# Kernel tuning notes

Hardware: AMD Instinct MI355X
Metric: run time of the kernel (lower is better)

Reference implementation:

```python
import jax, jax.numpy as jnp
import numpy as np

NUM_HEADS = 12
HEAD_DIM = 64
HIDDEN = NUM_HEADS * HEAD_DIM
SCALE = 1.0 / float(np.sqrt(HEAD_DIM))


def _split_heads(x):
    # x: [b, d, s, hidden] -> [b, h, d, s, head_dim]  (transpose_for_scores)
    b, d, s, _ = x.shape
    return jnp.transpose(x.reshape(b, d, s, NUM_HEADS, HEAD_DIM), (0, 3, 1, 2, 4))


def _merge_heads(x):
    # [b, h, d, s, e] -> [b, d, s, hidden]  (untranspose_for_scores)
    b, h, d, s, e = x.shape
    return jnp.transpose(x, (0, 2, 3, 1, 4)).reshape(b, d, s, h * e)


def _segment_attention(q, keys, values, masks, num_docs):
    # _cat_forward: broadcast every key/value/mask list entry to num_docs along
    # dim 2, concat along key length, then scaled-dot-product attention.
    b, h = q.shape[0], q.shape[1]
    q = jnp.broadcast_to(q, (b, h, num_docs, q.shape[3], q.shape[4]))
    k = jnp.concatenate([jnp.broadcast_to(t, (b, h, num_docs, t.shape[3], t.shape[4])) for t in keys], axis=3)
    v = jnp.concatenate([jnp.broadcast_to(t, (b, h, num_docs, t.shape[3], t.shape[4])) for t in values], axis=3)
    mask = jnp.concatenate([jnp.broadcast_to(m, (b, 1, num_docs, 1, m.shape[-1])) for m in masks], axis=-1)
    scores = jnp.einsum('bhdqe,bhdke->bhdqk', q, k) * SCALE + mask
    probs = jax.nn.softmax(scores, axis=-1)
    ctx = jnp.einsum('bhdqk,bhdke->bhdqe', probs, v)
    return _merge_heads(ctx)


def setup_inputs() -> dict:
    key = jax.random.key(0)
    ks = jax.random.split(key, 8)
    B, D, Q, S = 2, 16, 32, 512
    inp = {
        'cls': jax.random.normal(ks[0], (B, 1, 1, HIDDEN), jnp.float32),
        'query': jax.random.normal(ks[1], (B, 1, Q, HIDDEN), jnp.float32),
        'doc': jax.random.normal(ks[2], (B, D, S, HIDDEN), jnp.float32),
        'qmask': jnp.zeros((B, 1, 1, 1, Q), jnp.float32),
        'dmask': jnp.zeros((B, 1, D, 1, S), jnp.float32),
        'Wq': jax.random.normal(ks[3], (HIDDEN, HIDDEN), jnp.float32) * 0.02,
        'bq': jnp.zeros((HIDDEN,), jnp.float32),
        'Wk': jax.random.normal(ks[4], (HIDDEN, HIDDEN), jnp.float32) * 0.02,
        'bk': jnp.zeros((HIDDEN,), jnp.float32),
        'Wv': jax.random.normal(ks[5], (HIDDEN, HIDDEN), jnp.float32) * 0.02,
        'bv': jnp.zeros((HIDDEN,), jnp.float32),
    }
    return inp


def reference(cls, query, doc, qmask, dmask, Wq, bq, Wk, bk, Wv, bv):
    num_docs = doc.shape[1]
    b = cls.shape[0]
    # per-segment q/k/v projections + head split
    segs = {}
    for name, hs in (('cls', cls), ('query', query), ('doc', doc)):
        segs[name] = tuple(_split_heads(hs @ W.T + bb) for W, bb in ((Wq, bq), (Wk, bk), (Wv, bv)))
    cmask = jnp.zeros((b, 1, 1, 1, cls.shape[2]), cls.dtype)  # cls token never padded
    masks = {'cls': cmask, 'query': qmask, 'doc': dmask}
    names = ('cls', 'query', 'doc')
    keys = [segs[n][1] for n in names]
    vals = [segs[n][2] for n in names]
    mlist = [masks[n] for n in names]
    # all segment->segment attention flags default True; attention_window_size
    # is None so each segment goes through the _cat_forward path
    outs = [_segment_attention(segs[n][0], keys, vals, mlist, num_docs) for n in names]
    # cls:[b,D,1,H], query:[b,D,Q,H], doc:[b,D,S,H] -> concat along seq for one output
    return jnp.concatenate(outs, axis=2)
```

## Files before the change

kernel.cpp:

```cpp
#include <hip/hip_runtime.h>
#include <hip/hip_bf16.h>

#define NH      12
#define HD      64
#define HID     768
#define B_      2
#define D_      16
#define QL      32
#define SL      512
#define SEQ     545
#define RPB     8225
#define TOT_ROWS 16450
#define PAD_ROWS 16512
#define VT_R    8256
#define WSZ     589824
#define SCALE_  0.125f
#define LOG2E   1.4426950408889634f
#define QSF     0.18033688011112042f

typedef __attribute__((ext_vector_type(8))) short short8;
typedef __attribute__((ext_vector_type(4))) short short4v;
typedef __attribute__((ext_vector_type(4))) float float4v;
typedef __attribute__((ext_vector_type(2))) unsigned int uint2v;

__device__ __forceinline__ short f2bf(float f) {
    __hip_bfloat16 h = __float2bfloat16(f);
    short s; __builtin_memcpy(&s, &h, 2);
    return s;
}

__device__ __forceinline__ unsigned int cvtpk(float a, float b) {
    unsigned int r;
    asm("v_cvt_pk_bf16_f32 %0, %1, %2" : "=v"(r) : "v"(a), "v"(b));
    return r;
}

__device__ __forceinline__ void gl2lds16(const short* g, short* l) {
    __builtin_amdgcn_global_load_lds(
        (const __attribute__((address_space(1))) void*)g,
        (__attribute__((address_space(3))) void*)l, 16, 0, 0);
}

#define PACK_BLKS  12384
#define WPACK_BLKS 1728

__global__ __launch_bounds__(256) void pack_all(
    const float* __restrict__ cls, const float* __restrict__ query,
    const float* __restrict__ doc,
    const float* __restrict__ Wq, const float* __restrict__ Wk,
    const float* __restrict__ Wv,
    short* __restrict__ X, short* __restrict__ Wb)
{
    int bid = blockIdx.x;
    if (bid < PACK_BLKS) {
        int idx = (bid * 256 + threadIdx.x) * 4;
        int row = idx / HID;
        int col = idx - row * HID;
        float4 v = make_float4(0.f, 0.f, 0.f, 0.f);
        if (row < TOT_ROWS) {
            int b = row / RPB;
            int r = row - b * RPB;
            const float* src;
            if (r == 0)        src = cls   + b * HID + col;
            else if (r < 33)   src = query + ((size_t)(b * QL + (r - 1))) * HID + col;
            else               src = doc   + ((size_t)(b * (D_ * SL) + (r - 33))) * HID + col;
            v = *reinterpret_cast<const float4*>(src);
        }
        short4v o;
        o[0] = f2bf(v.x); o[1] = f2bf(v.y); o[2] = f2bf(v.z); o[3] = f2bf(v.w);
        *reinterpret_cast<short4v*>(X + idx) = o;
    } else {
        int idx = ((bid - PACK_BLKS) * 256 + threadIdx.x) * 4;
        int z = idx / WSZ;
        int r = idx - z * WSZ;
        const float* src = (z == 0 ? Wq : (z == 1 ? Wk : Wv)) + r;
        float sc = (z == 0) ? QSF : 1.0f;
        float4 v = *reinterpret_cast<const float4*>(src);
        short4v o;
        o[0] = f2bf(v.x * sc); o[1] = f2bf(v.y * sc);
        o[2] = f2bf(v.z * sc); o[3] = f2bf(v.w * sc);
        *reinterpret_cast<short4v*>(Wb + idx) = o;
    }
}

__global__ __launch_bounds__(256) void proj4u(
    const short* __restrict__ X, const short* __restrict__ Wb,
    const float* __restrict__ bq, const float* __restrict__ bk,
    const float* __restrict__ bv,
    short* __restrict__ Qb, short* __restrict__ Kb, short* __restrict__ Vt)
{
    __shared__ short Xs[2][128 * 64];
    __shared__ short Ws[2][128 * 64];

    int tid = threadIdx.x, lane = tid & 63, wave = tid >> 6;

    int lin = blockIdx.x + 18 * blockIdx.y;
    {
        const int q = 290, r = 2;
        int xcd = lin & 7, seq = lin >> 3;
        lin = (xcd < r ? xcd * (q + 1) : r * (q + 1) + (xcd - r) * q) + seq;
    }
    int mblk = lin / 18;
    int nz   = lin - mblk * 18;
    int zi   = nz % 3;
    int nblk = nz / 3;
    bool vsw = (zi == 2);
    const short* W = Wb + (size_t)zi * WSZ;
    int m0 = mblk * 128, n0 = nblk * 128;

    int moff = (wave & 1) * 64, noff = (wave >> 1) * 64;
    int lr = lane & 15, lg = lane >> 4;

    const short* xsrc[4];
    const short* wsrc[4];
#pragma unroll
    for (int p = 0; p < 4; ++p) {
        int s = p * 256 + tid;
        int row = s >> 3, c = s & 7;
        int col = (c ^ (row & 7)) * 8;
        xsrc[p] = X + (size_t)(m0 + row) * HID + col;
        wsrc[p] = W + (size_t)(n0 + row) * HID + col;
    }

    float4v acc[4][4];
    for (int mi = 0; mi < 4; ++mi)
        for (int ni = 0; ni < 4; ++ni)
            acc[mi][ni] = (float4v){0.f, 0.f, 0.f, 0.f};

#define PSTAGE(bufi, kt) do {                                               \
    _Pragma("unroll")                                                       \
    for (int p = 0; p < 4; ++p) {                                           \
        gl2lds16(xsrc[p] + (kt) * 64,                                       \
                 &Xs[bufi][(p * 256 + (tid & 0xC0)) * 8]);                  \
        gl2lds16(wsrc[p] + (kt) * 64,                                       \
                 &Ws[bufi][(p * 256 + (tid & 0xC0)) * 8]);                  \
    } } while (0)

    PSTAGE(0, 0);
#pragma unroll
    for (int kt = 0; kt < 12; ++kt) {
        __syncthreads();
        if (kt < 11) PSTAGE((kt + 1) & 1, kt + 1);
        const short* xb = Xs[kt & 1];
        const short* wb = Ws[kt & 1];
        short8 afl[4], afh[4], bfl[4], bfh[4];
        for (int mi = 0; mi < 4; ++mi) {
            int r = moff + mi * 16 + lr;
            int x0 = lg ^ (r & 7);
            afl[mi] = *reinterpret_cast<const short8*>(&xb[r * 64 + x0 * 8]);
            afh[mi] = *reinterpret_cast<const short8*>(&xb[r * 64 + (x0 ^ 4) * 8]);
        }
        for (int ni = 0; ni < 4; ++ni) {
            int r = noff + ni * 16 + lr;
            int x0 = lg ^ (r & 7);
            bfl[ni] = *reinterpret_cast<const short8*>(&wb[r * 64 + x0 * 8]);
            bfh[ni] = *reinterpret_cast<const short8*>(&wb[r * 64 + (x0 ^ 4) * 8]);
        }
        if (!vsw) {
            for (int mi = 0; mi < 4; ++mi)
                for (int ni = 0; ni < 4; ++ni) {
                    acc[mi][ni] = __builtin_amdgcn_mfma_f32_16x16x32_bf16(
                        afl[mi], bfl[ni], acc[mi][ni], 0, 0, 0);
                    acc[mi][ni] = __builtin_amdgcn_mfma_f32_16x16x32_bf16(
                        afh[mi], bfh[ni], acc[mi][ni], 0, 0, 0);
                }
        } else {
            for (int mi = 0; mi < 4; ++mi)
                for (int ni = 0; ni < 4; ++ni) {
                    acc[mi][ni] = __builtin_amdgcn_mfma_f32_16x16x32_bf16(
                        bfl[ni], afl[mi], acc[mi][ni], 0, 0, 0);
                    acc[mi][ni] = __builtin_amdgcn_mfma_f32_16x16x32_bf16(
                        bfh[ni], afh[mi], acc[mi][ni], 0, 0, 0);
                }
        }
    }
#undef PSTAGE

    if (!vsw) {
        short* Y = zi == 0 ? Qb : Kb;
        const float* bias = zi == 0 ? bq : bk;
        float bsc = zi == 0 ? QSF : 1.0f;
        for (int ni = 0; ni < 4; ++ni) {
            int gcol = n0 + noff + ni * 16 + lr;
            float bb = bias[gcol] * bsc;
            for (int mi = 0; mi < 4; ++mi) {
                int growb = m0 + moff + mi * 16 + lg * 4;
                for (int r = 0; r < 4; ++r)
                    Y[(size_t)(growb + r) * HID + gcol] = f2bf(acc[mi][ni][r] + bb);
            }
        }
    } else {
        for (int ni = 0; ni < 4; ++ni) {
            float4 b4 = *reinterpret_cast<const float4*>(&bv[n0 + noff + ni * 16 + lg * 4]);
            const float* bbr = reinterpret_cast<const float*>(&b4);
            for (int mi = 0; mi < 4; ++mi) {
                int grow = m0 + moff + mi * 16 + lr;
                if (grow >= TOT_ROWS) continue;
                int b  = grow >= RPB ? 1 : 0;
                int rb = grow - b * RPB;
                int vr = rb < 33 ? rb : rb + 7;
                size_t cb = ((size_t)(b * HID + n0 + noff + ni * 16 + lg * 4)) * VT_R;
                for (int r = 0; r < 4; ++r)
                    Vt[cb + (size_t)r * VT_R + vr] = f2bf(acc[mi][ni][r] + bbr[r]);
            }
        }
    }
}

__device__ __forceinline__ int row_of(int b, int d, int t) {
    t = t > 544 ? 544 : t;
    int base = b * RPB;
    if (t < 512)  return base + 33 + d * SL + t;
    if (t == 512) return base;
    return base + (t - 512);
}

__global__ __launch_bounds__(256) void attn4(
    const short* __restrict__ Qb, const short* __restrict__ Kb,
    const short* __restrict__ Vt,
    const float* __restrict__ qmask, const float* __restrict__ dmask,
    float* __restrict__ out)
{
    __shared__ short Ks[2][64 * 64];
    __shared__ short Vs[2][64 * 64];
    __shared__ float maskv[576];

    int tid  = threadIdx.x;
    int lane = tid & 63, wave = tid >> 6;

    int lin = blockIdx.x + 5 * blockIdx.y;
    {
        int xcd = lin & 7, seq = lin >> 3;
        lin = xcd * 240 + seq;
    }
    int hbd = lin / 5;
    int qc  = lin - hbd * 5;
    int h = hbd >> 5, bd = hbd & 31;
    int b = bd >> 4, d = bd & 15;

    int lr = lane & 15, lg = lane >> 4, lk = lg * 8;
    int base = b * RPB;
    const short* vbase = Vt + (size_t)(b * HID + h * HD) * VT_R;

#define ASTAGE(bufi, kt) do {                                               \
    for (int p = 0; p < 2; ++p) {                                           \
        int s2 = p * 256 + tid;                                             \
        int r = s2 >> 3, c = s2 & 7;                                        \
        const short* g = Kb + (size_t)row_of(b, d, (kt) * 64 + r) * HID     \
                       + h * HD + ((c ^ (r & 7)) * 8);                      \
        gl2lds16(g, &Ks[bufi][(p * 256 + (tid & 0xC0)) * 8]);               \
    }                                                                       \
    for (int p = 0; p < 2; ++p) {                                           \
        int s2 = p * 256 + tid;                                             \
        int rd = s2 >> 3, c = s2 & 7;                                       \
        int tc = (kt) * 64 + ((c ^ (rd & 7)) * 8);                          \
        int vr = tc < 512 ? 40 + d * SL + tc : tc - 512;                    \
        gl2lds16(vbase + (size_t)rd * VT_R + vr,                            \
                 &Vs[bufi][(p * 256 + (tid & 0xC0)) * 8]);                  \
    } } while (0)

    ASTAGE(0, 0);

    for (int i = tid; i < 576; i += 256) {
        float mv;
        if (i < 512)       mv = dmask[(size_t)(b * D_ + d) * SL + i];
        else if (i == 512) mv = 0.f;
        else if (i < 545)  mv = qmask[b * QL + (i - 513)];
        else               mv = -INFINITY;
        maskv[i] = mv * LOG2E;
    }

    short8 bq0[2], bq1[2];
    for (int s = 0; s < 2; ++s) {
        int qtok = qc * 128 + s * 64 + wave * 16 + lr;
        int qrow = qtok < 512 ? base + 33 + d * SL + qtok : base + qtok - 512;
        const short* qp = Qb + (size_t)qrow * HID + h * HD + lk;
        bq0[s] = *reinterpret_cast<const short8*>(qp);
        bq1[s] = *reinterpret_cast<const short8*>(qp + 32);
    }

    float m_i[2] = {-1e30f, -1e30f};
    float lp[2]  = {0.f, 0.f};
    float4v o[2][4];
    for (int s = 0; s < 2; ++s)
        for (int nt = 0; nt < 4; ++nt) o[s][nt] = (float4v){0.f, 0.f, 0.f, 0.f};

#pragma unroll
    for (int kt = 0; kt < 9; ++kt) {
        __syncthreads();
        if (kt < 8) ASTAGE((kt + 1) & 1, kt + 1);
        const short* kb = Ks[kt & 1];
        const short* vbuf = Vs[kt & 1];

        short8 kf0[4], kf1[4];
        for (int nt = 0; nt < 4; ++nt) {
            int r = nt * 16 + lr;
            int x0 = lg ^ (r & 7);
            kf0[nt] = *reinterpret_cast<const short8*>(&kb[r * 64 + x0 * 8]);
            kf1[nt] = *reinterpret_cast<const short8*>(&kb[r * 64 + (x0 ^ 4) * 8]);
        }

        for (int s = 0; s < 2; ++s) {
            float p4[4][4];
            __builtin_amdgcn_s_setprio(1);
            for (int nt = 0; nt < 4; ++nt) {
                float4v z = *reinterpret_cast<const float4v*>(
                    &maskv[kt * 64 + nt * 16 + lg * 4]);
                z = __builtin_amdgcn_mfma_f32_16x16x32_bf16(kf0[nt], bq0[s], z, 0, 0, 0);
                z = __builtin_amdgcn_mfma_f32_16x16x32_bf16(kf1[nt], bq1[s], z, 0, 0, 0);
                for (int r = 0; r < 4; ++r) p4[nt][r] = z[r];
            }
            __builtin_amdgcn_s_setprio(0);

            float c0 = fmaxf(fmaxf(p4[0][0], p4[0][1]), p4[0][2]);
            float c1 = fmaxf(fmaxf(p4[0][3], p4[1][0]), p4[1][1]);
            float c2 = fmaxf(fmaxf(p4[1][2], p4[1][3]), p4[2][0]);
            float c3 = fmaxf(fmaxf(p4[2][1], p4[2][2]), p4[2][3]);
            float c4 = fmaxf(fmaxf(p4[3][0], p4[3][1]), p4[3][2]);
            float lmax = fmaxf(fmaxf(fmaxf(c0, c1), fmaxf(c2, c3)),
                               fmaxf(c4, p4[3][3]));

            if (__any(lmax > m_i[s] + 8.0f)) {
                float tmx = fmaxf(lmax, __shfl_xor(lmax, 16));
                tmx = fmaxf(tmx, __shfl_xor(tmx, 32));
                float mnew = fmaxf(m_i[s], tmx);
                float alpha = exp2f(m_i[s] - mnew);
                m_i[s] = mnew;
                lp[s] *= alpha;
                float al[4];
                for (int r = 0; r < 4; ++r) al[r] = __shfl(alpha, lg * 4 + r);
                for (int nt = 0; nt < 4; ++nt)
                    for (int r = 0; r < 4; ++r) o[s][nt][r] *= al[r];
            }

            for (int nt = 0; nt < 4; ++nt)
                for (int r = 0; r < 4; ++r)
                    p4[nt][r] = exp2f(p4[nt][r] - m_i[s]);
            float s0 = (p4[0][0] + p4[0][1]) + (p4[0][2] + p4[0][3]);
            float s1 = (p4[1][0] + p4[1][1]) + (p4[1][2] + p4[1][3]);
            float s2 = (p4[2][0] + p4[2][1]) + (p4[2][2] + p4[2][3]);
            float s3 = (p4[3][0] + p4[3][1]) + (p4[3][2] + p4[3][3]);
            lp[s] += (s0 + s1) + (s2 + s3);

            unsigned int wa[4], wbv[4];
            for (int nt = 0; nt < 4; ++nt) {
                wa[nt]  = cvtpk(p4[nt][0], p4[nt][1]);
                wbv[nt] = cvtpk(p4[nt][2], p4[nt][3]);
            }
            uint2v tA01 = __builtin_amdgcn_permlane32_swap(wa[0],  wa[1],  false, false);
            uint2v uA01 = __builtin_amdgcn_permlane16_swap(tA01[0], tA01[1], false, false);
            uint2v tB01 = __builtin_amdgcn_permlane32_swap(wbv[0], wbv[1], false, false);
            uint2v uB01 = __builtin_amdgcn_permlane16_swap(tB01[0], tB01[1], false, false);
            uint2v tA23 = __builtin_amdgcn_permlane32_swap(wa[2],  wa[3],  false, false);
            uint2v uA23 = __builtin_amdgcn_permlane16_swap(tA23[0], tA23[1], false, false);
            uint2v tB23 = __builtin_amdgcn_permlane32_swap(wbv[2], wbv[3], false, false);
            uint2v uB23 = __builtin_amdgcn_permlane16_swap(tB23[0], tB23[1], false, false);

            union { unsigned int u[4]; short8 s8; } A0, A1;
            A0.u[0] = uA01[0]; A0.u[1] = uB01[0]; A0.u[2] = uA01[1]; A0.u[3] = uB01[1];
            A1.u[0] = uA23[0]; A1.u[1] = uB23[0]; A1.u[2] = uA23[1]; A1.u[3] = uB23[1];
            short8 ap0 = A0.s8;
            short8 ap1 = A1.s8;

            __builtin_amdgcn_s_setprio(1);
            for (int nt = 0; nt < 4; ++nt) {
                int rd = nt * 16 + lr;
                int x0 = lg ^ (rd & 7);
                short8 bv0 = *reinterpret_cast<const short8*>(&vbuf[rd * 64 + x0 * 8]);
                short8 bv1 = *reinterpret_cast<const short8*>(&vbuf[rd * 64 + (x0 ^ 4) * 8]);
                o[s][nt] = __builtin_amdgcn_mfma_f32_16x16x32_bf16(ap0, bv0, o[s][nt], 0, 0, 0);
                o[s][nt] = __builtin_amdgcn_mfma_f32_16x16x32_bf16(ap1, bv1, o[s][nt], 0, 0, 0);
            }
            __builtin_amdgcn_s_setprio(0);
        }
    }
#undef ASTAGE

    for (int s = 0; s < 2; ++s) {
        float lt = lp[s];
        lt += __shfl_xor(lt, 16);
        lt += __shfl_xor(lt, 32);
        float li[4];
        for (int r = 0; r < 4; ++r) li[r] = __shfl(lt, lg * 4 + r);
        for (int r = 0; r < 4; ++r) {
            int t = qc * 128 + s * 64 + wave * 16 + lg * 4 + r;
            if (t >= SEQ) continue;
            int seq = t < 512 ? 33 + t : (t == 512 ? 0 : t - 512);
            float inv = 1.f / li[r];
            float* op = out + ((size_t)(bd * SEQ + seq)) * HID + h * HD + lr;
            for (int nt = 0; nt < 4; ++nt)
                op[nt * 16] = o[s][nt][r] * inv;
        }
    }
}

extern "C" void kernel_launch(void* const* d_in, const int* in_sizes, int n_in,
                              void* d_out, int out_size, void* d_ws, size_t ws_size,
                              hipStream_t stream)
{
    const float* cls   = (const float*)d_in[0];
    const float* query = (const float*)d_in[1];
    const float* doc   = (const float*)d_in[2];
    const float* qmask = (const float*)d_in[3];
    const float* dmask = (const float*)d_in[4];
    const float* Wq = (const float*)d_in[5];
    const float* bq = (const float*)d_in[6];
    const float* Wk = (const float*)d_in[7];
    const float* bk = (const float*)d_in[8];
    const float* Wv = (const float*)d_in[9];
    const float* bv = (const float*)d_in[10];
    float* out = (float*)d_out;

    short* X  = (short*)d_ws;
    size_t seg = (size_t)PAD_ROWS * HID;
    short* Qb = X + seg;
    short* Kb = Qb + seg;
    short* Vt = Kb + seg;
    short* Wb = (short*)d_out;

    pack_all<<<dim3(PACK_BLKS + WPACK_BLKS), 256, 0, stream>>>(
        cls, query, doc, Wq, Wk, Wv, X, Wb);
    proj4u<<<dim3(18, 129, 1), 256, 0, stream>>>(X, Wb, bq, bk, bv, Qb, Kb, Vt);
    attn4<<<dim3(5, NH * 32, 1), 256, 0, stream>>>(Qb, Kb, Vt, qmask, dmask, out);
}
```

Baseline: 285.4 us.

## Triple-buffer attention K/V staging and widen query tiles to three subtiles per wave

The attention kernel goes from double to triple-buffered K/V LDS staging. It waits on explicit vmcnt counts and issues a single barrier per iteration, so loads run two tiles ahead. Each block now handles 192 query tokens (3 subtiles per wave) instead of 128, so K/V tiles are reused across more queries and the grid shrinks from 5 to 3 chunks per head/doc. Global addresses are precomputed once instead of recomputing row_of each stage, and mask loads are hoisted out of the subtile loop. The cost is more registers and LDS per block, which may lower occupancy, and fewer blocks in the grid.

```diff
diff --git a/kernel.cpp b/kernel.cpp
--- a/kernel.cpp
+++ b/kernel.cpp
@@ -207,34 +207,26 @@
     }
 }
 
-__device__ __forceinline__ int row_of(int b, int d, int t) {
-    t = t > 544 ? 544 : t;
-    int base = b * RPB;
-    if (t < 512)  return base + 33 + d * SL + t;
-    if (t == 512) return base;
-    return base + (t - 512);
-}
-
-__global__ __launch_bounds__(256) void attn4(
+__global__ __launch_bounds__(256) void attn5(
     const short* __restrict__ Qb, const short* __restrict__ Kb,
     const short* __restrict__ Vt,
     const float* __restrict__ qmask, const float* __restrict__ dmask,
     float* __restrict__ out)
 {
-    __shared__ short Ks[2][64 * 64];
-    __shared__ short Vs[2][64 * 64];
+    __shared__ short Ks[3][64 * 64];
+    __shared__ short Vs[3][64 * 64];
     __shared__ float maskv[576];
 
     int tid  = threadIdx.x;
     int lane = tid & 63, wave = tid >> 6;
 
-    int lin = blockIdx.x + 5 * blockIdx.y;
+    int lin = blockIdx.x + 3 * blockIdx.y;
     {
         int xcd = lin & 7, seq = lin >> 3;
-        lin = xcd * 240 + seq;
-    }
-    int hbd = lin / 5;
-    int qc  = lin - hbd * 5;
+        lin = xcd * 144 + seq;
+    }
+    int hbd = lin / 3;
+    int qc  = lin - hbd * 3;
     int h = hbd >> 5, bd = hbd & 31;
     int b = bd >> 4, d = bd & 15;
 
@@ -242,24 +234,35 @@
     int base = b * RPB;
     const short* vbase = Vt + (size_t)(b * HID + h * HD) * VT_R;
 
-#define ASTAGE(bufi, kt) do {                                               \
-    for (int p = 0; p < 2; ++p) {                                           \
-        int s2 = p * 256 + tid;                                             \
-        int r = s2 >> 3, c = s2 & 7;                                        \
-        const short* g = Kb + (size_t)row_of(b, d, (kt) * 64 + r) * HID     \
-                       + h * HD + ((c ^ (r & 7)) * 8);                      \
-        gl2lds16(g, &Ks[bufi][(p * 256 + (tid & 0xC0)) * 8]);               \
-    }                                                                       \
-    for (int p = 0; p < 2; ++p) {                                           \
-        int s2 = p * 256 + tid;                                             \
-        int rd = s2 >> 3, c = s2 & 7;                                       \
-        int tc = (kt) * 64 + ((c ^ (rd & 7)) * 8);                          \
-        int vr = tc < 512 ? 40 + d * SL + tc : tc - 512;                    \
-        gl2lds16(vbase + (size_t)rd * VT_R + vr,                            \
-                 &Vs[bufi][(p * 256 + (tid & 0xC0)) * 8]);                  \
-    } } while (0)
-
-    ASTAGE(0, 0);
+    const short* kp[2]; const short* vp[2];
+    const short* kp8[2]; const short* vp8[2];
+    int loff[2];
+#pragma unroll
+    for (int p = 0; p < 2; ++p) {
+        int s2 = p * 256 + tid;
+        int r = s2 >> 3, c = s2 & 7;
+        int colsw = (c ^ (r & 7)) * 8;
+        kp[p] = Kb + (size_t)(base + 33 + d * SL + r) * HID + h * HD + colsw;
+        vp[p] = vbase + (size_t)r * VT_R + 40 + d * SL + colsw;
+        int r8 = r > 32 ? 32 : r;
+        kp8[p] = Kb + (size_t)(base + r8) * HID + h * HD + colsw;
+        vp8[p] = vbase + (size_t)r * VT_R + colsw;
+        loff[p] = (p * 256 + (tid & 0xC0)) * 8;
+    }
+
+#define ALIN(bufi, kt) do {                                       \
+    gl2lds16(kp[0] + (size_t)(kt) * 64 * HID, &Ks[bufi][loff[0]]);\
+    gl2lds16(kp[1] + (size_t)(kt) * 64 * HID, &Ks[bufi][loff[1]]);\
+    gl2lds16(vp[0] + (kt) * 64, &Vs[bufi][loff[0]]);              \
+    gl2lds16(vp[1] + (kt) * 64, &Vs[bufi][loff[1]]); } while (0)
+#define A8(bufi) do {                                             \
+    gl2lds16(kp8[0], &Ks[bufi][loff[0]]);                         \
+    gl2lds16(kp8[1], &Ks[bufi][loff[1]]);                         \
+    gl2lds16(vp8[0], &Vs[bufi][loff[0]]);                         \
+    gl2lds16(vp8[1], &Vs[bufi][loff[1]]); } while (0)
+
+    ALIN(0, 0);
+    ALIN(1, 1);
 
     for (int i = tid; i < 576; i += 256) {
         float mv;
@@ -270,42 +273,56 @@
         maskv[i] = mv * LOG2E;
     }
 
-    short8 bq0[2], bq1[2];
-    for (int s = 0; s < 2; ++s) {
-        int qtok = qc * 128 + s * 64 + wave * 16 + lr;
+    short8 bq0[3], bq1[3];
+#pragma unroll
+    for (int s = 0; s < 3; ++s) {
+        int qtok = qc * 192 + s * 64 + wave * 16 + lr;
         int qrow = qtok < 512 ? base + 33 + d * SL + qtok : base + qtok - 512;
         const short* qp = Qb + (size_t)qrow * HID + h * HD + lk;
         bq0[s] = *reinterpret_cast<const short8*>(qp);
         bq1[s] = *reinterpret_cast<const short8*>(qp + 32);
     }
 
-    float m_i[2] = {-1e30f, -1e30f};
-    float lp[2]  = {0.f, 0.f};
-    float4v o[2][4];
-    for (int s = 0; s < 2; ++s)
+    float m_i[3] = {-1e30f, -1e30f, -1e30f};
+    float lp[3]  = {0.f, 0.f, 0.f};
+    float4v o[3][4];
+    for (int s = 0; s < 3; ++s)
         for (int nt = 0; nt < 4; ++nt) o[s][nt] = (float4v){0.f, 0.f, 0.f, 0.f};
 
+    __syncthreads();
+
 #pragma unroll
     for (int kt = 0; kt < 9; ++kt) {
-        __syncthreads();
-        if (kt < 8) ASTAGE((kt + 1) & 1, kt + 1);
-        const short* kb = Ks[kt & 1];
-        const short* vbuf = Vs[kt & 1];
-
+        if (kt >= 1) {
+            if (kt == 8) { asm volatile("s_waitcnt vmcnt(0)" ::: "memory"); }
+            else         { asm volatile("s_waitcnt vmcnt(4)" ::: "memory"); }
+            __builtin_amdgcn_s_barrier();
+            __builtin_amdgcn_sched_barrier(0);
+        }
+        if (kt < 6)       ALIN((kt + 2) % 3, kt + 2);
+        else if (kt == 6) A8((kt + 2) % 3);
+
+        const short* kb   = Ks[kt % 3];
+        const short* vbuf = Vs[kt % 3];
+
+        float4v mk[4];
         short8 kf0[4], kf1[4];
+#pragma unroll
         for (int nt = 0; nt < 4; ++nt) {
+            mk[nt] = *reinterpret_cast<const float4v*>(
+                &maskv[kt * 64 + nt * 16 + lg * 4]);
             int r = nt * 16 + lr;
             int x0 = lg ^ (r & 7);
             kf0[nt] = *reinterpret_cast<const short8*>(&kb[r * 64 + x0 * 8]);
             kf1[nt] = *reinterpret_cast<const short8*>(&kb[r * 64 + (x0 ^ 4) * 8]);
         }
 
-        for (int s = 0; s < 2; ++s) {
+#pragma unroll
+        for (int s = 0; s < 3; ++s) {
             float p4[4][4];
             __builtin_amdgcn_s_setprio(1);
             for (int nt = 0; nt < 4; ++nt) {
-                float4v z = *reinterpret_cast<const float4v*>(
-                    &maskv[kt * 64 + nt * 16 + lg * 4]);
+                float4v z = mk[nt];
                 z = __builtin_amdgcn_mfma_f32_16x16x32_bf16(kf0[nt], bq0[s], z, 0, 0, 0);
                 z = __builtin_amdgcn_mfma_f32_16x16x32_bf16(kf1[nt], bq1[s], z, 0, 0, 0);
                 for (int r = 0; r < 4; ++r) p4[nt][r] = z[r];
@@ -374,16 +391,17 @@
             __builtin_amdgcn_s_setprio(0);
         }
     }
-#undef ASTAGE
-
-    for (int s = 0; s < 2; ++s) {
+#undef ALIN
+#undef A8
+
+    for (int s = 0; s < 3; ++s) {
         float lt = lp[s];
         lt += __shfl_xor(lt, 16);
         lt += __shfl_xor(lt, 32);
         float li[4];
         for (int r = 0; r < 4; ++r) li[r] = __shfl(lt, lg * 4 + r);
         for (int r = 0; r < 4; ++r) {
-            int t = qc * 128 + s * 64 + wave * 16 + lg * 4 + r;
+            int t = qc * 192 + s * 64 + wave * 16 + lg * 4 + r;
             if (t >= SEQ) continue;
             int seq = t < 512 ? 33 + t : (t == 512 ? 0 : t - 512);
             float inv = 1.f / li[r];
@@ -421,5 +439,5 @@
     pack_all<<<dim3(PACK_BLKS + WPACK_BLKS), 256, 0, stream>>>(
         cls, query, doc, Wq, Wk, Wv, X, Wb);
     proj4u<<<dim3(18, 129, 1), 256, 0, stream>>>(X, Wb, bq, bk, bv, Qb, Kb, Vt);
-    attn4<<<dim3(5, NH * 32, 1), 256, 0, stream>>>(Qb, Kb, Vt, qmask, dmask, out);
-}
+    attn5<<<dim3(3, NH * 32, 1), 256, 0, stream>>>(Qb, Kb, Vt, qmask, dmask, out);
+}
```

Measured after the change: 278.3 us. 1.03x faster.
